# Kernel tuning notes

Measured on AMD Instinct MI355X. Metric: run time of the kernel, lower is better.

The kernel has to match this reference:

```python
import jax, jax.numpy as jnp
import numpy as np

EMBED = 1024
HEADS = 16


def setup_inputs() -> dict:
    key = jax.random.key(0)
    ks = jax.random.split(key, 12)
    N, S, E = 8, 1024, EMBED
    s = 1.0 / np.sqrt(E)
    inp = {
        'queries': jax.random.normal(ks[0], (N, S, E), jnp.float32),
        'keys': jax.random.normal(ks[1], (N, S, E), jnp.float32),
        'values': jax.random.normal(ks[2], (N, S, E), jnp.float32),
        'Wq': jax.random.normal(ks[3], (E, E), jnp.float32) * s,
        'bq': jax.random.normal(ks[4], (E,), jnp.float32) * s,
        'Wk': jax.random.normal(ks[5], (E, E), jnp.float32) * s,
        'bk': jax.random.normal(ks[6], (E,), jnp.float32) * s,
        'Wv': jax.random.normal(ks[7], (E, E), jnp.float32) * s,
        'bv': jax.random.normal(ks[8], (E,), jnp.float32) * s,
        'Wo': jax.random.normal(ks[9], (E, E), jnp.float32) * s,
        'bo': jax.random.normal(ks[10], (E,), jnp.float32) * s,
    }
    return inp


def reference(queries, keys, values, Wq, bq, Wk, bk, Wv, bv, Wo, bo):
    N, S, E = queries.shape
    H = HEADS
    D = E // H
    # linear projections (torch Linear: x @ W.T + b)
    q = queries @ Wq.T + bq
    k = keys @ Wk.T + bk
    v = values @ Wv.T + bv
    q = q.reshape(N, S, H, D)
    k = k.reshape(N, S, H, D)
    v = v.reshape(N, S, H, D)
    # NOTE: original scales by sqrt(embed_size), not sqrt(head_dim)
    scores = jnp.einsum('nqhd,nkhd->nhqk', q, k) / jnp.sqrt(jnp.float32(E))
    attn = jax.nn.softmax(scores, axis=3)
    out = jnp.einsum('nhqk,nkhd->nqhd', attn, v).reshape(N, S, E)
    return out @ Wo.T + bo
```

## Files before the change

kernel.cpp:

```cpp
#include <hip/hip_runtime.h>


typedef unsigned short ushort_t;
typedef __bf16 bf16_8 __attribute__((ext_vector_type(8)));
typedef float f32x4 __attribute__((ext_vector_type(4)));
typedef unsigned short ushort8 __attribute__((ext_vector_type(8)));
typedef short short8v __attribute__((ext_vector_type(8)));

#define SEQ  1024
#define EMB  1024
#define NBAT 8
#define NH   16
#define HD   64
#define MROW (NBAT * SEQ)

__device__ __forceinline__ ushort_t cvt_bf16(float x) {
  unsigned u = __float_as_uint(x);
  u += 0x7FFFu + ((u >> 16) & 1u);
  return (ushort_t)(u >> 16);
}
__device__ __forceinline__ float bf2f(ushort_t u) {
  return __uint_as_float(((unsigned)u) << 16);
}
__device__ __forceinline__ short f2bs(float x) {
  return __builtin_bit_cast(short, (__bf16)x);
}

__device__ __forceinline__ void async_copy16(const ushort_t* g, ushort_t* l) {
  __builtin_amdgcn_global_load_lds(
      (const __attribute__((address_space(1))) void*)g,
      (__attribute__((address_space(3))) void*)l, 16, 0, 0);
}

__global__ void dtype_probe(const ushort_t* __restrict__ w, int* __restrict__ flag) {
  __shared__ int cnt;
  if (threadIdx.x == 0) cnt = 0;
  __syncthreads();
  int c = 0;
  for (int i = threadIdx.x; i < 4096; i += 256) {
    const int e = (w[i] >> 7) & 0xFF;
    if (e >= 129) ++c;
  }
  atomicAdd(&cnt, c);
  __syncthreads();
  if (threadIdx.x == 0) *flag = (cnt > 256) ? 1 : 0;
}

__device__ __forceinline__ ushort8 load8(const void* base, size_t off, bool f32) {
  if (f32) {
    const float* p = (const float*)base + off;
    const f32x4 a = *(const f32x4*)p;
    const f32x4 b = *(const f32x4*)(p + 4);
    ushort8 r;
    r[0] = cvt_bf16(a[0]); r[1] = cvt_bf16(a[1]);
    r[2] = cvt_bf16(a[2]); r[3] = cvt_bf16(a[3]);
    r[4] = cvt_bf16(b[0]); r[5] = cvt_bf16(b[1]);
    r[6] = cvt_bf16(b[2]); r[7] = cvt_bf16(b[3]);
    return r;
  }
  return *(const ushort8*)((const ushort_t*)base + off);
}

__global__ __launch_bounds__(256)
void convert_all(const void* __restrict__ q, const void* __restrict__ k,
                 const void* __restrict__ v, const void* __restrict__ wq,
                 const void* __restrict__ wk, const void* __restrict__ wv,
                 const void* __restrict__ wo,
                 ushort_t* __restrict__ cq, ushort_t* __restrict__ ck,
                 ushort_t* __restrict__ cv, ushort_t* __restrict__ cwq,
                 ushort_t* __restrict__ cwk, ushort_t* __restrict__ cwv,
                 ushort_t* __restrict__ cwo, const int* __restrict__ flag) {
  const bool f32 = (*flag != 0);
  const int b = blockIdx.x;
  const void* src;
  ushort_t* dst;
  int boff;
  if (b < 12288) {
    const int t = b >> 12;
    boff = b & 4095;
    src = (t == 0) ? q : (t == 1) ? k : v;
    dst = (t == 0) ? cq : (t == 1) ? ck : cv;
  } else {
    const int t = (b - 12288) >> 9;
    boff = (b - 12288) & 511;
    src = (t == 0) ? wq : (t == 1) ? wk : (t == 2) ? wv : wo;
    dst = (t == 0) ? cwq : (t == 1) ? cwk : (t == 2) ? cwv : cwo;
  }
  const size_t i = (size_t)boff * 256 + threadIdx.x;
  *(ushort8*)(dst + i * 8) = load8(src, i * 8, f32);
}

__device__ __forceinline__ void gemm_body(
    const ushort_t* __restrict__ A, const ushort_t* __restrict__ B,
    const void* __restrict__ bias, void* __restrict__ Cout, bool f32, int bid,
    int scatter, int final_out) {
  __shared__ __align__(16) ushort_t As[128 * 32];
  __shared__ __align__(16) ushort_t Bs[128 * 32];
  const int tid  = threadIdx.x;
  const int lane = tid & 63;
  const int wave = tid >> 6;
  const int wm = wave & 1, wn = wave >> 1;
  const int col  = lane & 15;
  const int quad = lane >> 4;
  const int bm = (bid & 63) << 7;
  const int bn = (bid >> 6) << 7;

  const ushort_t* Ab = A + (size_t)bm * EMB;
  const ushort_t* Bb = B + (size_t)bn * EMB;

  float bvv[4];
#pragma unroll
  for (int nt = 0; nt < 4; ++nt) {
    const int i = bn + wn * 64 + nt * 16 + col;
    bvv[nt] = f32 ? ((const float*)bias)[i] : bf2f(((const ushort_t*)bias)[i]);
  }

  f32x4 acc[4][4] = {};

  for (int kb = 0; kb < EMB; kb += 32) {
#pragma unroll
    for (int j = 0; j < 2; ++j) {
      const int s   = j * 256 + tid;
      const int row = s >> 2;
      const int ch  = (s & 3) << 3;
      const int s0  = j * 256 + wave * 64;
      async_copy16(Ab + (size_t)row * EMB + kb + ch, &As[s0 * 8]);
      async_copy16(Bb + (size_t)row * EMB + kb + ch, &Bs[s0 * 8]);
    }
    __syncthreads();

    bf16_8 af[4], bfr[4];
#pragma unroll
    for (int mt = 0; mt < 4; ++mt)
      af[mt] = *(const bf16_8*)(As + (wm * 64 + mt * 16 + col) * 32 + quad * 8);
#pragma unroll
    for (int nt = 0; nt < 4; ++nt)
      bfr[nt] = *(const bf16_8*)(Bs + (wn * 64 + nt * 16 + col) * 32 + quad * 8);
#pragma unroll
    for (int mt = 0; mt < 4; ++mt)
#pragma unroll
      for (int nt = 0; nt < 4; ++nt)
        acc[mt][nt] = __builtin_amdgcn_mfma_f32_16x16x32_bf16(af[mt], bfr[nt],
                                                              acc[mt][nt], 0, 0, 0);
    __syncthreads();
  }

#pragma unroll
  for (int mt = 0; mt < 4; ++mt)
#pragma unroll
    for (int nt = 0; nt < 4; ++nt) {
      const int gcol = bn + wn * 64 + nt * 16 + col;
#pragma unroll
      for (int r = 0; r < 4; ++r) {
        const int grow = bm + wm * 64 + mt * 16 + quad * 4 + r;
        const float vv = acc[mt][nt][r] + bvv[nt];
        if (!scatter) {
          const size_t idx = (size_t)grow * EMB + gcol;
          if (final_out && f32) ((float*)Cout)[idx] = vv;
          else                  ((ushort_t*)Cout)[idx] = cvt_bf16(vv);
        } else {
          const int nn = grow >> 10, ss = grow & 1023;
          const int hh = gcol >> 6,  dd = gcol & 63;
          ((ushort_t*)Cout)[(size_t)((nn * NH + hh) * HD + dd) * SEQ + ss] =
              cvt_bf16(vv);
        }
      }
    }
}

__global__ __launch_bounds__(256)
void gemm_qk(const ushort_t* __restrict__ cq, const ushort_t* __restrict__ ck,
             const ushort_t* __restrict__ cWq, const ushort_t* __restrict__ cWk,
             const void* __restrict__ bq, const void* __restrict__ bk,
             void* __restrict__ Qp, void* __restrict__ Kp,
             const int* __restrict__ flag) {
  const bool f32 = (*flag != 0);
  const int which = blockIdx.x >> 9;
  const int bid = blockIdx.x & 511;
  const ushort_t* A = which ? ck : cq;
  const ushort_t* B = which ? cWk : cWq;
  const void* bi    = which ? bk : bq;
  void* C           = which ? Kp : Qp;
  gemm_body(A, B, bi, C, f32, bid, 0, 0);
}

__global__ __launch_bounds__(256)
void gemm_one(const ushort_t* __restrict__ A, const ushort_t* __restrict__ B,
              const void* __restrict__ bias, void* __restrict__ Cout,
              const int* __restrict__ flag, int scatter, int final_out) {
  gemm_body(A, B, bias, Cout, (*flag != 0), blockIdx.x, scatter, final_out);
}

template <int MODE>
__global__ __launch_bounds__(256)
void gemm_flex(const void* __restrict__ A, const void* __restrict__ B,
               const void* __restrict__ bias, void* __restrict__ Cout,
               const int* __restrict__ flag, int a_ext, int final_out) {
  __shared__ __align__(16) ushort_t As[128 * 32];
  __shared__ __align__(16) ushort_t Bs[128 * 32];
  const bool f32  = (*flag != 0);
  const bool af32 = f32 && (a_ext != 0);
  const int tid  = threadIdx.x;
  const int lane = tid & 63;
  const int wave = tid >> 6;
  const int wm = wave & 1, wn = wave >> 1;
  const int col  = lane & 15;
  const int quad = lane >> 4;
  const int bm = (blockIdx.x & 63) << 7;
  const int bn = (blockIdx.x >> 6) << 7;

  f32x4 acc[4][4] = {};

  for (int kb = 0; kb < EMB; kb += 32) {
    ushort8 ra[2], rb[2];
#pragma unroll
    for (int j = 0; j < 2; ++j) {
      const int s   = j * 256 + tid;
      const int row = s >> 2;
      const int ch  = (s & 3) << 3;
      ra[j] = load8(A, (size_t)(bm + row) * EMB + kb + ch, af32);
      rb[j] = load8(B, (size_t)(bn + row) * EMB + kb + ch, f32);
    }
#pragma unroll
    for (int j = 0; j < 2; ++j) {
      const int s = j * 256 + tid;
      *(ushort8*)(As + s * 8) = ra[j];
      *(ushort8*)(Bs + s * 8) = rb[j];
    }
    __syncthreads();

    bf16_8 af[4], bfr[4];
#pragma unroll
    for (int mt = 0; mt < 4; ++mt)
      af[mt] = *(const bf16_8*)(As + (wm * 64 + mt * 16 + col) * 32 + quad * 8);
#pragma unroll
    for (int nt = 0; nt < 4; ++nt)
      bfr[nt] = *(const bf16_8*)(Bs + (wn * 64 + nt * 16 + col) * 32 + quad * 8);
#pragma unroll
    for (int mt = 0; mt < 4; ++mt)
#pragma unroll
      for (int nt = 0; nt < 4; ++nt)
        acc[mt][nt] = __builtin_amdgcn_mfma_f32_16x16x32_bf16(af[mt], bfr[nt],
                                                              acc[mt][nt], 0, 0, 0);
    __syncthreads();
  }

  float bvv[4];
#pragma unroll
  for (int nt = 0; nt < 4; ++nt) {
    const int i = bn + wn * 64 + nt * 16 + col;
    bvv[nt] = f32 ? ((const float*)bias)[i] : bf2f(((const ushort_t*)bias)[i]);
  }
#pragma unroll
  for (int mt = 0; mt < 4; ++mt)
#pragma unroll
    for (int nt = 0; nt < 4; ++nt) {
      const int gcol = bn + wn * 64 + nt * 16 + col;
#pragma unroll
      for (int r = 0; r < 4; ++r) {
        const int grow = bm + wm * 64 + mt * 16 + quad * 4 + r;
        const float vv = acc[mt][nt][r] + bvv[nt];
        if (MODE == 0) {
          const size_t idx = (size_t)grow * EMB + gcol;
          if (final_out && f32) ((float*)Cout)[idx] = vv;
          else                  ((ushort_t*)Cout)[idx] = cvt_bf16(vv);
        } else {
          const int nn = grow >> 10, ss = grow & 1023;
          const int hh = gcol >> 6,  dd = gcol & 63;
          ((ushort_t*)Cout)[(size_t)((nn * NH + hh) * HD + dd) * SEQ + ss] =
              cvt_bf16(vv);
        }
      }
    }
}

__global__ __launch_bounds__(256)
void attn_kernel(const ushort_t* __restrict__ Q, const ushort_t* __restrict__ K,
                 const ushort_t* __restrict__ V, ushort_t* __restrict__ O) {
  const int tid  = threadIdx.x;
  const int lane = tid & 63;
  const int wave = tid >> 6;
  const int col  = lane & 15;
  const int quad = lane >> 4;
  const int gid = blockIdx.x;
  const int nh  = gid & 127;
  const int qb  = gid >> 7;
  const int h  = nh & 15;
  const int n  = nh >> 4;
  const int q0 = qb * 128 + wave * 32;

  bf16_8 aq0[2], aq1[2];
#pragma unroll
  for (int g = 0; g < 2; ++g) {
    const ushort_t* qp =
        Q + (size_t)(n * SEQ + q0 + g * 16 + col) * EMB + h * HD + quad * 8;
    aq0[g] = *(const bf16_8*)qp;
    aq1[g] = *(const bf16_8*)(qp + 32);
  }

  const int sig = ((col >> 2) << 3) | (col & 3);
  const ushort_t* kp = K + (size_t)(n * SEQ + sig) * EMB + h * HD + quad * 8;
  const ushort_t* vp = V + ((size_t)nh * HD + col) * SEQ + quad * 8;

  f32x4 acc[2][4] = {};
  float lsum[2] = {0.f, 0.f};

  const float SCL = 0.04508422f;
  const float MOF = 16.0f;

#define ATTN_LOAD(KX, VX, KB_)                                               \
  do {                                                                       \
    const ushort_t* kpi = kp + (size_t)(KB_) * EMB;                          \
    KX[0] = *(const bf16_8*)(kpi);                                           \
    KX[1] = *(const bf16_8*)(kpi + 32);                                      \
    KX[2] = *(const bf16_8*)(kpi + 4 * EMB);                                 \
    KX[3] = *(const bf16_8*)(kpi + 4 * EMB + 32);                            \
    _Pragma("unroll")                                                        \
    for (int dt = 0; dt < 4; ++dt)                                           \
      VX[dt] = *(const bf16_8*)(vp + (size_t)dt * 16 * SEQ + (KB_));         \
  } while (0)

#define ATTN_TILE(KX, VX)                                                    \
  do {                                                                       \
    _Pragma("unroll")                                                        \
    for (int g = 0; g < 2; ++g) {                                            \
      const f32x4 z = {};                                                    \
      __builtin_amdgcn_s_setprio(1);                                         \
      f32x4 s0 = __builtin_amdgcn_mfma_f32_16x16x32_bf16(KX[0], aq0[g], z, 0, 0, 0); \
      s0 = __builtin_amdgcn_mfma_f32_16x16x32_bf16(KX[1], aq1[g], s0, 0, 0, 0);      \
      f32x4 s1 = __builtin_amdgcn_mfma_f32_16x16x32_bf16(KX[2], aq0[g], z, 0, 0, 0); \
      s1 = __builtin_amdgcn_mfma_f32_16x16x32_bf16(KX[3], aq1[g], s1, 0, 0, 0);      \
      __builtin_amdgcn_s_setprio(0);                                         \
      short8v pas;                                                           \
      _Pragma("unroll")                                                      \
      for (int r = 0; r < 4; ++r) {                                          \
        const float p0 = exp2f(__builtin_fmaf(s0[r], SCL, -MOF));            \
        const float p1 = exp2f(__builtin_fmaf(s1[r], SCL, -MOF));            \
        lsum[g] += p0 + p1;                                                  \
        pas[r]     = f2bs(p0);                                               \
        pas[r + 4] = f2bs(p1);                                               \
      }                                                                      \
      const bf16_8 pab = __builtin_bit_cast(bf16_8, pas);                    \
      __builtin_amdgcn_s_setprio(1);                                         \
      _Pragma("unroll")                                                      \
      for (int dt = 0; dt < 4; ++dt)                                         \
        acc[g][dt] = __builtin_amdgcn_mfma_f32_16x16x32_bf16(pab, VX[dt], acc[g][dt], 0, 0, 0); \
      __builtin_amdgcn_s_setprio(0);                                         \
    }                                                                        \
  } while (0)

  bf16_8 KA[4], KB2[4], VA[4], VB[4];

  ATTN_LOAD(KA, VA, 0);
  for (int kb = 0; kb < SEQ; kb += 64) {
    ATTN_LOAD(KB2, VB, kb + 32);
    __builtin_amdgcn_sched_barrier(0);
    ATTN_TILE(KA, VA);
    if (kb + 64 < SEQ) {
      ATTN_LOAD(KA, VA, kb + 64);
      __builtin_amdgcn_sched_barrier(0);
    }
    ATTN_TILE(KB2, VB);
  }

#undef ATTN_LOAD
#undef ATTN_TILE

#pragma unroll
  for (int g = 0; g < 2; ++g) {
    float tot = lsum[g];
    tot += __shfl_xor(tot, 16, 64);
    tot += __shfl_xor(tot, 32, 64);
    float rinv[4];
#pragma unroll
    for (int r = 0; r < 4; ++r)
      rinv[r] = 1.0f / __shfl(tot, quad * 4 + r, 16);
#pragma unroll
    for (int dt = 0; dt < 4; ++dt)
#pragma unroll
      for (int r = 0; r < 4; ++r)
        O[(size_t)(n * SEQ + q0 + g * 16 + quad * 4 + r) * EMB + h * HD +
          dt * 16 + col] = cvt_bf16(acc[g][dt][r] * rinv[r]);
  }
}

extern "C" void kernel_launch(void* const* d_in, const int* in_sizes, int n_in,
                              void* d_out, int out_size, void* d_ws, size_t ws_size,
                              hipStream_t stream) {
  const void* q  = d_in[0];
  const void* k  = d_in[1];
  const void* v  = d_in[2];
  const void* Wq = d_in[3];
  const void* bq = d_in[4];
  const void* Wk = d_in[5];
  const void* bk = d_in[6];
  const void* Wv = d_in[7];
  const void* bv = d_in[8];
  const void* Wo = d_in[9];
  const void* bo = d_in[10];

  const size_t TE = (size_t)MROW * EMB;
  const size_t WE = (size_t)EMB * EMB;
  int* flag = (int*)d_ws;
  char* base = (char*)d_ws + 256;
  const size_t NEED = 256 + (4 * TE + 4 * WE) * sizeof(ushort_t);

  const dim3 tB(256);
  dtype_probe<<<dim3(1), tB, 0, stream>>>((const ushort_t*)Wq, flag);

  if (ws_size >= NEED) {
    ushort_t* cq  = (ushort_t*)base;
    ushort_t* ck  = cq + TE;
    ushort_t* cv  = ck + TE;
    ushort_t* Qp  = cv + TE;
    ushort_t* cWq = Qp + TE;
    ushort_t* cWk = cWq + WE;
    ushort_t* cWv = cWk + WE;
    ushort_t* cWo = cWv + WE;
    ushort_t* Kp  = (ushort_t*)d_out;
    ushort_t* Vt  = cq;
    ushort_t* Oa  = Qp;

    convert_all<<<dim3(14336), tB, 0, stream>>>(q, k, v, Wq, Wk, Wv, Wo,
                                                cq, ck, cv, cWq, cWk, cWv, cWo,
                                                flag);

    gemm_qk<<<dim3(1024), tB, 0, stream>>>(cq, ck, cWq, cWk, bq, bk, Qp, Kp, flag);
    gemm_one<<<dim3(512), tB, 0, stream>>>(cv, cWv, bv, Vt, flag, 1, 0);
    attn_kernel<<<dim3(1024), tB, 0, stream>>>(Qp, Kp, Vt, Oa);
    gemm_one<<<dim3(512), tB, 0, stream>>>(Oa, cWo, bo, d_out, flag, 0, 1);
  } else {
    ushort_t* Qp = (ushort_t*)base;
    ushort_t* Vt = Qp + TE;
    ushort_t* Kp = (ushort_t*)d_out;
    ushort_t* Oa = Qp;
    const dim3 gB(512);
    gemm_flex<0><<<gB, tB, 0, stream>>>(q, Wq, bq, Qp, flag, 1, 0);
    gemm_flex<0><<<gB, tB, 0, stream>>>(k, Wk, bk, Kp, flag, 1, 0);
    gemm_flex<1><<<gB, tB, 0, stream>>>(v, Wv, bv, Vt, flag, 1, 0);
    attn_kernel<<<dim3(1024), tB, 0, stream>>>(Qp, Kp, Vt, Oa);
    gemm_flex<0><<<gB, tB, 0, stream>>>(Oa, Wo, bo, d_out, flag, 0, 1);
  }
}
```

Baseline: 398.2 us.

## Fuse V projection into QKV GEMM, compute V transposed, and double attention rows per wave

The V projection moves into the combined Q/K GEMM launch as a third group of blocks. It computes W_v·v^T with a row-indexed bias so the transposed head layout is written with contiguous stores instead of a strided scatter. V^T now lives in the second half of the output buffer. Each attention wave handles 64 query rows instead of 32, so every K/V fragment is reused across twice as many rows on half as many blocks, and exp2f becomes the raw hardware exp2. This saves a launch and halves K/V traffic, but doubles accumulator registers, which may lower occupancy and leaves only 512 attention blocks.

```diff
diff --git a/kernel.cpp b/kernel.cpp
--- a/kernel.cpp
+++ b/kernel.cpp
@@ -91,28 +91,27 @@
 }
 
 __device__ __forceinline__ void gemm_body(
+    ushort_t* As, ushort_t* Bs,
     const ushort_t* __restrict__ A, const ushort_t* __restrict__ B,
-    const void* __restrict__ bias, void* __restrict__ Cout, bool f32, int bid,
-    int scatter, int final_out) {
-  __shared__ __align__(16) ushort_t As[128 * 32];
-  __shared__ __align__(16) ushort_t Bs[128 * 32];
+    const void* __restrict__ bias, void* __restrict__ Cout, bool f32,
+    int bm, int bn, int mode) {
   const int tid  = threadIdx.x;
   const int lane = tid & 63;
   const int wave = tid >> 6;
   const int wm = wave & 1, wn = wave >> 1;
   const int col  = lane & 15;
   const int quad = lane >> 4;
-  const int bm = (bid & 63) << 7;
-  const int bn = (bid >> 6) << 7;
 
   const ushort_t* Ab = A + (size_t)bm * EMB;
   const ushort_t* Bb = B + (size_t)bn * EMB;
 
   float bvv[4];
-#pragma unroll
-  for (int nt = 0; nt < 4; ++nt) {
-    const int i = bn + wn * 64 + nt * 16 + col;
-    bvv[nt] = f32 ? ((const float*)bias)[i] : bf2f(((const ushort_t*)bias)[i]);
+  if (mode != 1) {
+#pragma unroll
+    for (int nt = 0; nt < 4; ++nt) {
+      const int i = bn + wn * 64 + nt * 16 + col;
+      bvv[nt] = f32 ? ((const float*)bias)[i] : bf2f(((const ushort_t*)bias)[i]);
+    }
   }
 
   f32x4 acc[4][4] = {};
@@ -153,42 +152,53 @@
 #pragma unroll
       for (int r = 0; r < 4; ++r) {
         const int grow = bm + wm * 64 + mt * 16 + quad * 4 + r;
-        const float vv = acc[mt][nt][r] + bvv[nt];
-        if (!scatter) {
-          const size_t idx = (size_t)grow * EMB + gcol;
-          if (final_out && f32) ((float*)Cout)[idx] = vv;
-          else                  ((ushort_t*)Cout)[idx] = cvt_bf16(vv);
-        } else {
-          const int nn = grow >> 10, ss = grow & 1023;
-          const int hh = gcol >> 6,  dd = gcol & 63;
+        if (mode == 1) {
+          const float bb =
+              f32 ? ((const float*)bias)[grow] : bf2f(((const ushort_t*)bias)[grow]);
+          const float vv = acc[mt][nt][r] + bb;
+          const int nn = gcol >> 10, ss = gcol & 1023;
+          const int hh = grow >> 6,  dd = grow & 63;
           ((ushort_t*)Cout)[(size_t)((nn * NH + hh) * HD + dd) * SEQ + ss] =
               cvt_bf16(vv);
+        } else {
+          const float vv = acc[mt][nt][r] + bvv[nt];
+          const size_t idx = (size_t)grow * EMB + gcol;
+          if (mode == 2 && f32) ((float*)Cout)[idx] = vv;
+          else                  ((ushort_t*)Cout)[idx] = cvt_bf16(vv);
         }
       }
     }
 }
 
 __global__ __launch_bounds__(256)
-void gemm_qk(const ushort_t* __restrict__ cq, const ushort_t* __restrict__ ck,
-             const ushort_t* __restrict__ cWq, const ushort_t* __restrict__ cWk,
-             const void* __restrict__ bq, const void* __restrict__ bk,
-             void* __restrict__ Qp, void* __restrict__ Kp,
-             const int* __restrict__ flag) {
+void gemm_qkv(const ushort_t* __restrict__ cq, const ushort_t* __restrict__ ck,
+              const ushort_t* __restrict__ cv, const ushort_t* __restrict__ cWq,
+              const ushort_t* __restrict__ cWk, const ushort_t* __restrict__ cWv,
+              const void* __restrict__ bq, const void* __restrict__ bk,
+              const void* __restrict__ bv, void* __restrict__ Qp,
+              void* __restrict__ Kp, void* __restrict__ Vt,
+              const int* __restrict__ flag) {
+  __shared__ __align__(16) ushort_t As[128 * 32];
+  __shared__ __align__(16) ushort_t Bs[128 * 32];
   const bool f32 = (*flag != 0);
-  const int which = blockIdx.x >> 9;
+  const int t = blockIdx.x >> 9;
   const int bid = blockIdx.x & 511;
-  const ushort_t* A = which ? ck : cq;
-  const ushort_t* B = which ? cWk : cWq;
-  const void* bi    = which ? bk : bq;
-  void* C           = which ? Kp : Qp;
-  gemm_body(A, B, bi, C, f32, bid, 0, 0);
+  if (t == 0)
+    gemm_body(As, Bs, cq, cWq, bq, Qp, f32, (bid & 63) << 7, (bid >> 6) << 7, 0);
+  else if (t == 1)
+    gemm_body(As, Bs, ck, cWk, bk, Kp, f32, (bid & 63) << 7, (bid >> 6) << 7, 0);
+  else
+    gemm_body(As, Bs, cWv, cv, bv, Vt, f32, (bid & 7) << 7, (bid >> 3) << 7, 1);
 }
 
 __global__ __launch_bounds__(256)
 void gemm_one(const ushort_t* __restrict__ A, const ushort_t* __restrict__ B,
               const void* __restrict__ bias, void* __restrict__ Cout,
-              const int* __restrict__ flag, int scatter, int final_out) {
-  gemm_body(A, B, bias, Cout, (*flag != 0), blockIdx.x, scatter, final_out);
+              const int* __restrict__ flag, int mode) {
+  __shared__ __align__(16) ushort_t As[128 * 32];
+  __shared__ __align__(16) ushort_t Bs[128 * 32];
+  gemm_body(As, Bs, A, B, bias, Cout, (*flag != 0),
+            (blockIdx.x & 63) << 7, (blockIdx.x >> 6) << 7, mode);
 }
 
 template <int MODE>
@@ -287,11 +297,11 @@
   const int qb  = gid >> 7;
   const int h  = nh & 15;
   const int n  = nh >> 4;
-  const int q0 = qb * 128 + wave * 32;
-
-  bf16_8 aq0[2], aq1[2];
-#pragma unroll
-  for (int g = 0; g < 2; ++g) {
+  const int q0 = qb * 256 + wave * 64;
+
+  bf16_8 aq0[4], aq1[4];
+#pragma unroll
+  for (int g = 0; g < 4; ++g) {
     const ushort_t* qp =
         Q + (size_t)(n * SEQ + q0 + g * 16 + col) * EMB + h * HD + quad * 8;
     aq0[g] = *(const bf16_8*)qp;
@@ -302,8 +312,8 @@
   const ushort_t* kp = K + (size_t)(n * SEQ + sig) * EMB + h * HD + quad * 8;
   const ushort_t* vp = V + ((size_t)nh * HD + col) * SEQ + quad * 8;
 
-  f32x4 acc[2][4] = {};
-  float lsum[2] = {0.f, 0.f};
+  f32x4 acc[4][4] = {};
+  float lsum[4] = {0.f, 0.f, 0.f, 0.f};
 
   const float SCL = 0.04508422f;
   const float MOF = 16.0f;
@@ -323,7 +333,7 @@
 #define ATTN_TILE(KX, VX)                                                    \
   do {                                                                       \
     _Pragma("unroll")                                                        \
-    for (int g = 0; g < 2; ++g) {                                            \
+    for (int g = 0; g < 4; ++g) {                                            \
       const f32x4 z = {};                                                    \
       __builtin_amdgcn_s_setprio(1);                                         \
       f32x4 s0 = __builtin_amdgcn_mfma_f32_16x16x32_bf16(KX[0], aq0[g], z, 0, 0, 0); \
@@ -334,8 +344,8 @@
       short8v pas;                                                           \
       _Pragma("unroll")                                                      \
       for (int r = 0; r < 4; ++r) {                                          \
-        const float p0 = exp2f(__builtin_fmaf(s0[r], SCL, -MOF));            \
-        const float p1 = exp2f(__builtin_fmaf(s1[r], SCL, -MOF));            \
+        const float p0 = __builtin_amdgcn_exp2f(__builtin_fmaf(s0[r], SCL, -MOF)); \
+        const float p1 = __builtin_amdgcn_exp2f(__builtin_fmaf(s1[r], SCL, -MOF)); \
         lsum[g] += p0 + p1;                                                  \
         pas[r]     = f2bs(p0);                                               \
         pas[r + 4] = f2bs(p1);                                               \
@@ -367,7 +377,7 @@
 #undef ATTN_TILE
 
 #pragma unroll
-  for (int g = 0; g < 2; ++g) {
+  for (int g = 0; g < 4; ++g) {
     float tot = lsum[g];
     tot += __shfl_xor(tot, 16, 64);
     tot += __shfl_xor(tot, 32, 64);
@@ -418,17 +428,16 @@
     ushort_t* cWv = cWk + WE;
     ushort_t* cWo = cWv + WE;
     ushort_t* Kp  = (ushort_t*)d_out;
-    ushort_t* Vt  = cq;
+    ushort_t* Vt  = (ushort_t*)d_out + TE;
     ushort_t* Oa  = Qp;
 
     convert_all<<<dim3(14336), tB, 0, stream>>>(q, k, v, Wq, Wk, Wv, Wo,
                                                 cq, ck, cv, cWq, cWk, cWv, cWo,
                                                 flag);
-
-    gemm_qk<<<dim3(1024), tB, 0, stream>>>(cq, ck, cWq, cWk, bq, bk, Qp, Kp, flag);
-    gemm_one<<<dim3(512), tB, 0, stream>>>(cv, cWv, bv, Vt, flag, 1, 0);
-    attn_kernel<<<dim3(1024), tB, 0, stream>>>(Qp, Kp, Vt, Oa);
-    gemm_one<<<dim3(512), tB, 0, stream>>>(Oa, cWo, bo, d_out, flag, 0, 1);
+    gemm_qkv<<<dim3(1536), tB, 0, stream>>>(cq, ck, cv, cWq, cWk, cWv,
+                                            bq, bk, bv, Qp, Kp, Vt, flag);
+    attn_kernel<<<dim3(512), tB, 0, stream>>>(Qp, Kp, Vt, Oa);
+    gemm_one<<<dim3(512), tB, 0, stream>>>(Oa, cWo, bo, d_out, flag, 2);
   } else {
     ushort_t* Qp = (ushort_t*)base;
     ushort_t* Vt = Qp + TE;
@@ -438,7 +447,7 @@
     gemm_flex<0><<<gB, tB, 0, stream>>>(q, Wq, bq, Qp, flag, 1, 0);
     gemm_flex<0><<<gB, tB, 0, stream>>>(k, Wk, bk, Kp, flag, 1, 0);
     gemm_flex<1><<<gB, tB, 0, stream>>>(v, Wv, bv, Vt, flag, 1, 0);
-    attn_kernel<<<dim3(1024), tB, 0, stream>>>(Qp, Kp, Vt, Oa);
+    attn_kernel<<<dim3(512), tB, 0, stream>>>(Qp, Kp, Vt, Oa);
     gemm_flex<0><<<gB, tB, 0, stream>>>(Oa, Wo, bo, d_out, flag, 0, 1);
   }
 }
```

Result: faster. 332.4 us (-16.5%).
